# Kernel optimization log

Hardware: AMD Instinct MI355X
Metric: run time of the kernel (lower is better)

Reference implementation:

```python
import jax, jax.numpy as jnp
import numpy as np

B, P, DIN, DK, H = 16, 1024, 768, 768, 12
HD = DK // H
NCLS = 1000


def setup_inputs() -> dict:
    key = jax.random.key(0)
    ks = jax.random.split(key, 7)
    s = 0.02
    return {
        "x": jax.random.normal(ks[0], (B, P, DIN), dtype=jnp.float32),
        "Wqkv": jax.random.normal(ks[1], (DIN, 3 * DK), dtype=jnp.float32) * s,
        "pos": jax.random.normal(ks[2], (1, P, DK), dtype=jnp.float32) * s,
        "Wo": jax.random.normal(ks[3], (DK, DK), dtype=jnp.float32) * s,
        "bo": jax.random.normal(ks[4], (DK,), dtype=jnp.float32) * s,
        "Wc": jax.random.normal(ks[5], (DK, NCLS), dtype=jnp.float32) * s,
        "bc": jax.random.normal(ks[6], (NCLS,), dtype=jnp.float32) * s,
    }


def reference(x, Wqkv, pos, Wo, bo, Wc, bc):
    qkv = x @ Wqkv  # [B,P,3*DK]
    Q, K, V = jnp.split(qkv, 3, axis=-1)
    Q, K, V = Q + pos, K + pos, V + pos

    def heads(t):  # [B,P,DK] -> [B,H,P,HD]
        return t.reshape(B, P, H, HD).transpose(0, 2, 1, 3)

    Q, K, V = heads(Q), heads(K), heads(V)
    scores = jnp.einsum('bhqd,bhkd->bhqk', Q, K) / jnp.sqrt(jnp.float32(HD))
    attn_weights = jax.nn.softmax(scores, axis=-1)
    attn_out = jnp.einsum('bhqk,bhkd->bhqd', attn_weights, V)
    attn_out = attn_out.transpose(0, 2, 1, 3).reshape(B, P, DK)
    attn_out = attn_out @ Wo + bo
    pooled = attn_out.mean(axis=1)  # [B,DK]
    logits = pooled @ Wc + bc
    return logits, attn_weights
```

## Files before the change

### kernel.cpp

```cpp
#include <hip/hip_runtime.h>

#define DI __device__ __forceinline__

typedef float f32x4 __attribute__((ext_vector_type(4)));
typedef unsigned short u16;
typedef u16 u16x8 __attribute__((ext_vector_type(8)));
typedef u16 u16x4 __attribute__((ext_vector_type(4)));
typedef __bf16 bf16x8 __attribute__((ext_vector_type(8)));

DI u16 f2bf(float f) {
    unsigned u = __builtin_bit_cast(unsigned, f);
    u += 0x7fffu + ((u >> 16) & 1u);
    return (u16)(u >> 16);
}

DI float bf2f(u16 b) {
    unsigned u = ((unsigned)b) << 16;
    return __builtin_bit_cast(float, u);
}

DI f32x4 mfma_bf16(u16x8 a, u16x8 b, f32x4 c) {
    return __builtin_amdgcn_mfma_f32_16x16x32_bf16(
        __builtin_bit_cast(bf16x8, a), __builtin_bit_cast(bf16x8, b), c, 0, 0, 0);
}

DI void gload_lds16(const void* g, void* l) {
    __builtin_amdgcn_global_load_lds(
        (const __attribute__((address_space(1))) unsigned int*)g,
        (__attribute__((address_space(3))) unsigned int*)l, 16, 0, 0);
}

DI float fast_exp2(float x) {
    float e;
    asm("v_exp_f32 %0, %1" : "=v"(e) : "v"(x));
    return e;
}

__global__ __launch_bounds__(256) void k_cast_x(const float* __restrict__ x, u16* __restrict__ xb) {
    size_t i = (size_t)blockIdx.x * 256 + threadIdx.x;
    const f32x4* p = (const f32x4*)(x + i * 8);
    f32x4 a = p[0], b = p[1];
    u16x8 o;
    o[0] = f2bf(a[0]); o[1] = f2bf(a[1]); o[2] = f2bf(a[2]); o[3] = f2bf(a[3]);
    o[4] = f2bf(b[0]); o[5] = f2bf(b[1]); o[6] = f2bf(b[2]); o[7] = f2bf(b[3]);
    *(u16x8*)(xb + i * 8) = o;
}

__global__ __launch_bounds__(256) void k_transpose_w(const float* __restrict__ W, u16* __restrict__ Wt) {
    __shared__ float tile[64][65];
    const int t = threadIdx.x;
    const int nb = blockIdx.x * 64, kb = blockIdx.y * 64;
#pragma unroll
    for (int it = 0; it < 4; ++it) {
        int idx = it * 256 + t;
        int kl = idx >> 4, nl4 = (idx & 15) * 4;
        f32x4 v = *(const f32x4*)(W + (size_t)(kb + kl) * 2304 + nb + nl4);
        tile[kl][nl4 + 0] = v[0]; tile[kl][nl4 + 1] = v[1];
        tile[kl][nl4 + 2] = v[2]; tile[kl][nl4 + 3] = v[3];
    }
    __syncthreads();
#pragma unroll
    for (int it = 0; it < 2; ++it) {
        int idx = it * 256 + t;
        int nl = idx >> 3, kc = (idx & 7) * 8;
        u16x8 o;
#pragma unroll
        for (int j = 0; j < 8; ++j) o[j] = f2bf(tile[kc + j][nl]);
        *(u16x8*)(Wt + (size_t)(nb + nl) * 768 + kb + kc) = o;
    }
}

__global__ __launch_bounds__(256, 2) void k_qkv(const u16* __restrict__ A, const u16* __restrict__ Bt,
                                                const float* __restrict__ pos, u16* __restrict__ Qb,
                                                u16* __restrict__ Kb, u16* __restrict__ Vt) {
    __shared__ __align__(16) union SM {
        u16 stage[2][2][8192];
        u16 vt[128][136];
    } sm;
    const int tid = threadIdx.x;
    const int l = tid & 63, w = tid >> 6;
    const int wm = w >> 1, wn = w & 1;
    const int m0 = blockIdx.x * 128, n0 = blockIdx.y * 128;
    const int srow = l >> 3, sslot = (l & 7) ^ srow;
    const int q4 = l >> 4, lr = l & 15;

    f32x4 acc[4][4];
#pragma unroll
    for (int i = 0; i < 4; ++i)
#pragma unroll
        for (int j = 0; j < 4; ++j) acc[i][j] = (f32x4){0.f, 0.f, 0.f, 0.f};

    const size_t abase = (size_t)(m0 + srow) * 768 + sslot * 8;
    const size_t bbase = (size_t)(n0 + srow) * 768 + sslot * 8;

#pragma unroll
    for (int i = 0; i < 4; ++i) {
        int chunk = w * 4 + i;
        gload_lds16(A + abase + (size_t)chunk * 8 * 768, &sm.stage[0][0][chunk * 512]);
        gload_lds16(Bt + bbase + (size_t)chunk * 8 * 768, &sm.stage[0][1][chunk * 512]);
    }
    __syncthreads();

    int cur = 0;
    for (int kt = 0; kt < 12; ++kt) {
        if (kt < 11) {
            const size_t ko = (size_t)(kt + 1) * 64;
#pragma unroll
            for (int i = 0; i < 4; ++i) {
                int chunk = w * 4 + i;
                gload_lds16(A + abase + (size_t)chunk * 8 * 768 + ko, &sm.stage[cur ^ 1][0][chunk * 512]);
                gload_lds16(Bt + bbase + (size_t)chunk * 8 * 768 + ko, &sm.stage[cur ^ 1][1][chunk * 512]);
            }
        }
        const u16* ab = sm.stage[cur][0];
        const u16* bb = sm.stage[cur][1];
        u16x8 af[4][2], bf[4][2];
#pragma unroll
        for (int mi = 0; mi < 4; ++mi) {
            int row = wm * 64 + mi * 16 + lr;
#pragma unroll
            for (int ks = 0; ks < 2; ++ks) {
                int kc = ks * 4 + q4;
                af[mi][ks] = *(const u16x8*)(ab + row * 64 + (kc ^ (row & 7)) * 8);
            }
        }
#pragma unroll
        for (int ni = 0; ni < 4; ++ni) {
            int row = wn * 64 + ni * 16 + lr;
#pragma unroll
            for (int ks = 0; ks < 2; ++ks) {
                int kc = ks * 4 + q4;
                bf[ni][ks] = *(const u16x8*)(bb + row * 64 + (kc ^ (row & 7)) * 8);
            }
        }
#pragma unroll
        for (int mi = 0; mi < 4; ++mi)
#pragma unroll
            for (int ni = 0; ni < 4; ++ni) {
                acc[mi][ni] = mfma_bf16(af[mi][0], bf[ni][0], acc[mi][ni]);
                acc[mi][ni] = mfma_bf16(af[mi][1], bf[ni][1], acc[mi][ni]);
            }
        __syncthreads();
        cur ^= 1;
    }

    const int sec = blockIdx.y / 6;
    const int dsec = n0 - sec * 768;
    const int bidx = m0 >> 10;
    const int prow = m0 & 1023;
    if (sec < 2) {
        u16* outp = sec ? Kb : Qb;
#pragma unroll
        for (int mi = 0; mi < 4; ++mi)
#pragma unroll
            for (int ni = 0; ni < 4; ++ni) {
                const int dl = wn * 64 + ni * 16 + lr;
                const int d = dsec + dl;
#pragma unroll
                for (int r = 0; r < 4; ++r) {
                    const int pl = wm * 64 + mi * 16 + q4 * 4 + r;
                    const int p = prow + pl;
                    sm.vt[pl][dl] = f2bf(acc[mi][ni][r] + pos[p * 768 + d]);
                }
            }
        __syncthreads();
#pragma unroll
        for (int it = 0; it < 8; ++it) {
            const int idx = it * 256 + tid;
            const int pl = idx >> 4, c8 = (idx & 15) * 8;
            u16x8 val = *(const u16x8*)(&sm.vt[pl][c8]);
            const int d = dsec + c8, h = d >> 6, hd = d & 63;
            *(u16x8*)(outp + (size_t)((bidx * 12 + h) * 1024 + prow + pl) * 64 + hd) = val;
        }
    } else {
#pragma unroll
        for (int mi = 0; mi < 4; ++mi)
#pragma unroll
            for (int ni = 0; ni < 4; ++ni) {
                int col = wn * 64 + ni * 16 + lr;
                int d = dsec + col;
                u16x4 pk;
#pragma unroll
                for (int r = 0; r < 4; ++r) {
                    int p = prow + wm * 64 + mi * 16 + q4 * 4 + r;
                    pk[r] = f2bf(acc[mi][ni][r] + pos[p * 768 + d]);
                }
                *(u16x4*)(&sm.vt[col][wm * 64 + mi * 16 + q4 * 4]) = pk;
            }
        __syncthreads();
#pragma unroll
        for (int it = 0; it < 8; ++it) {
            int idx = it * 256 + tid;
            int dl = idx >> 4, c8 = (idx & 15) * 8;
            u16x8 val = *(const u16x8*)(&sm.vt[dl][c8]);
            int d = dsec + dl, h = d >> 6, hd = d & 63;
            *(u16x8*)(Vt + (size_t)((bidx * 12 + h) * 64 + hd) * 1024 + prow + c8) = val;
        }
    }
}

__global__ __launch_bounds__(256, 4) void k_attn(const u16* __restrict__ Qb, const u16* __restrict__ Kb,
                                                 float* __restrict__ Pout, float* __restrict__ csws) {
    __shared__ float stats[64];
    const int tid = threadIdx.x;
    const int l = tid & 63, w = tid >> 6;
    const int lr = l & 15, q4 = l >> 4;
    const int bh = blockIdx.y, qb = blockIdx.x, q0 = qb * 16;
    const u16* Qh = Qb + (size_t)bh * 65536;
    const u16* Kh = Kb + (size_t)bh * 65536;

    u16x8 qf[2];
#pragma unroll
    for (int ks = 0; ks < 2; ++ks)
        qf[ks] = *(const u16x8*)(Qh + (size_t)(q0 + lr) * 64 + ks * 32 + q4 * 8);

    f32x4 acc[16];
#pragma unroll
    for (int nf = 0; nf < 16; ++nf) acc[nf] = (f32x4){0.f, 0.f, 0.f, 0.f};

    const int kc0 = w * 256;
#pragma unroll
    for (int nf = 0; nf < 16; ++nf) {
        const u16* kp = Kh + (size_t)(kc0 + nf * 16 + lr) * 64 + q4 * 8;
        u16x8 kf0 = *(const u16x8*)kp;
        u16x8 kf1 = *(const u16x8*)(kp + 32);
        acc[nf] = mfma_bf16(qf[0], kf0, acc[nf]);
        acc[nf] = mfma_bf16(qf[1], kf1, acc[nf]);
    }

    const float cs = 0.125f * 1.44269504f;
    float inv4[4];
#pragma unroll
    for (int r = 0; r < 4; ++r) {
        float s = 0.f;
#pragma unroll
        for (int nf = 0; nf < 16; ++nf) {
            float e = fast_exp2(acc[nf][r] * cs);
            acc[nf][r] = e;
            s += e;
        }
        s += __shfl_xor(s, 1);
        s += __shfl_xor(s, 2);
        s += __shfl_xor(s, 4);
        s += __shfl_xor(s, 8);
        if (lr == 0) stats[(q4 * 4 + r) * 4 + w] = s;
    }
    __syncthreads();
#pragma unroll
    for (int r = 0; r < 4; ++r) {
        f32x4 s4 = *(const f32x4*)(stats + (q4 * 4 + r) * 4);
        inv4[r] = 1.f / (s4[0] + s4[1] + s4[2] + s4[3]);
    }

    float* Prow = Pout + ((size_t)bh * 1024 + q0) * 1024 + kc0;
    float* crow = csws + ((size_t)(bh * 64 + qb)) * 1024 + kc0;
#pragma unroll
    for (int nf = 0; nf < 16; ++nf) {
        float csum = 0.f;
#pragma unroll
        for (int r = 0; r < 4; ++r) {
            const int row = q4 * 4 + r;
            float p = acc[nf][r] * inv4[r];
            __builtin_nontemporal_store(p, &Prow[(size_t)row * 1024 + nf * 16 + lr]);
            csum += p;
        }
        csum += __shfl_xor(csum, 16);
        csum += __shfl_xor(csum, 32);
        if (l < 16) crow[nf * 16 + l] = csum;
    }
}

__global__ __launch_bounds__(256) void k_pool(const float* __restrict__ csws, const u16* __restrict__ Vt,
                                              float* __restrict__ pooled) {
    __shared__ float cs[1024];
    __shared__ float ps[4][64];
    const int bh = blockIdx.x, t = threadIdx.x;
    f32x4 a = (f32x4){0.f, 0.f, 0.f, 0.f};
    const float* base = csws + (size_t)bh * 64 * 1024 + t * 4;
#pragma unroll 8
    for (int qb = 0; qb < 64; ++qb) a += *(const f32x4*)(base + qb * 1024);
    *(f32x4*)(cs + t * 4) = a;
    __syncthreads();
    const int d = t & 63, kc = t >> 6;
    const u16* vrow = Vt + (size_t)bh * 65536 + (size_t)d * 1024 + kc * 256;
    const float* ck = cs + kc * 256;
    float s = 0.f;
#pragma unroll
    for (int k8 = 0; k8 < 32; ++k8) {
        u16x8 v = *(const u16x8*)(vrow + k8 * 8);
#pragma unroll
        for (int j = 0; j < 8; ++j) s += ck[k8 * 8 + j] * bf2f(v[j]);
    }
    ps[kc][d] = s;
    __syncthreads();
    if (t < 64) {
        const int bb = bh / 12, hh = bh % 12;
        pooled[bb * 768 + hh * 64 + t] = ps[0][t] + ps[1][t] + ps[2][t] + ps[3][t];
    }
}

__global__ __launch_bounds__(128) void k_proj(const float* __restrict__ pooled_sum,
                                              const float* __restrict__ Wo, const float* __restrict__ bo,
                                              float* __restrict__ tmp) {
    const int b = blockIdx.y, j = blockIdx.x * 128 + threadIdx.x;
    __shared__ float pr[768];
    for (int i = threadIdx.x; i < 768; i += 128) pr[i] = pooled_sum[b * 768 + i] * (1.0f / 1024.0f);
    __syncthreads();
    float s = bo[j];
#pragma unroll 4
    for (int d = 0; d < 768; ++d) s = fmaf(pr[d], Wo[d * 768 + j], s);
    tmp[b * 768 + j] = s;
}

__global__ __launch_bounds__(128) void k_cls(const float* __restrict__ tmp,
                                             const float* __restrict__ Wc, const float* __restrict__ bc,
                                             float* __restrict__ out) {
    const int b = blockIdx.y, c = blockIdx.x * 128 + threadIdx.x;
    __shared__ float tr[768];
    for (int i = threadIdx.x; i < 768; i += 128) tr[i] = tmp[b * 768 + i];
    __syncthreads();
    if (c >= 1000) return;
    float s = bc[c];
#pragma unroll 4
    for (int j = 0; j < 768; ++j) s = fmaf(tr[j], Wc[j * 1000 + c], s);
    out[b * 1000 + c] = s;
}

extern "C" void kernel_launch(void* const* d_in, const int* in_sizes, int n_in,
                              void* d_out, int out_size, void* d_ws, size_t ws_size,
                              hipStream_t stream) {
    const float* x    = (const float*)d_in[0];
    const float* Wqkv = (const float*)d_in[1];
    const float* pos  = (const float*)d_in[2];
    const float* Wo   = (const float*)d_in[3];
    const float* bo   = (const float*)d_in[4];
    const float* Wc   = (const float*)d_in[5];
    const float* bc   = (const float*)d_in[6];
    float* out  = (float*)d_out;
    float* attn = out + 16000;

    char* ws = (char*)d_ws;
    u16* xb = (u16*)ws;  ws += (size_t)16384 * 768 * 2;
    u16* Wt = (u16*)ws;  ws += (size_t)2304 * 768 * 2;
    u16* Qb = (u16*)ws;  ws += (size_t)192 * 1024 * 64 * 2;
    u16* Kb = (u16*)ws;  ws += (size_t)192 * 1024 * 64 * 2;
    u16* Vt = (u16*)ws;  ws += (size_t)192 * 1024 * 64 * 2;
    float* csws = (float*)ws;  ws += (size_t)12288 * 1024 * sizeof(float);
    float* pooled = (float*)ws;  ws += 16 * 768 * sizeof(float);
    float* tmp = (float*)ws;

    k_cast_x<<<6144, 256, 0, stream>>>(x, xb);
    k_transpose_w<<<dim3(36, 12), 256, 0, stream>>>(Wqkv, Wt);
    k_qkv<<<dim3(128, 18), 256, 0, stream>>>(xb, Wt, pos, Qb, Kb, Vt);
    k_attn<<<dim3(64, 192), 256, 0, stream>>>(Qb, Kb, attn, csws);
    k_pool<<<192, 256, 0, stream>>>(csws, Vt, pooled);
    k_proj<<<dim3(6, 16), 128, 0, stream>>>(pooled, Wo, bo, tmp);
    k_cls<<<dim3(8, 16), 128, 0, stream>>>(tmp, Wc, bc, out);
}
```

Measured before the change: 447.6 us.

## Recompute QK scores in two passes to cut registers and raise attention occupancy

The attention kernel no longer keeps all 16 score fragments live. It computes QK^T in chunks of four fragments to get the row sums, then recomputes the scores in a second pass and normalizes by subtracting log2(sum) inside the exponent. This lowers register pressure so the launch bound can rise from 4 to 6 blocks per SM, which should help hide the latency of the large P stores. The cost is doubled MFMA work and doubled K loads, with a small change in numerics from the log-domain normalization.

```diff
diff --git a/kernel.cpp b/kernel.cpp
--- a/kernel.cpp
+++ b/kernel.cpp
@@ -33,6 +33,12 @@
 DI float fast_exp2(float x) {
     float e;
     asm("v_exp_f32 %0, %1" : "=v"(e) : "v"(x));
+    return e;
+}
+
+DI float fast_log2(float x) {
+    float e;
+    asm("v_log_f32 %0, %1" : "=v"(e) : "v"(x));
     return e;
 }
 
@@ -199,7 +205,7 @@
     }
 }
 
-__global__ __launch_bounds__(256, 4) void k_attn(const u16* __restrict__ Qb, const u16* __restrict__ Kb,
+__global__ __launch_bounds__(256, 6) void k_attn(const u16* __restrict__ Qb, const u16* __restrict__ Kb,
                                                  float* __restrict__ Pout, float* __restrict__ csws) {
     __shared__ float stats[64];
     const int tid = threadIdx.x;
@@ -208,37 +214,43 @@
     const int bh = blockIdx.y, qb = blockIdx.x, q0 = qb * 16;
     const u16* Qh = Qb + (size_t)bh * 65536;
     const u16* Kh = Kb + (size_t)bh * 65536;
+    const int kc0 = w * 256;
 
     u16x8 qf[2];
 #pragma unroll
     for (int ks = 0; ks < 2; ++ks)
         qf[ks] = *(const u16x8*)(Qh + (size_t)(q0 + lr) * 64 + ks * 32 + q4 * 8);
 
-    f32x4 acc[16];
-#pragma unroll
-    for (int nf = 0; nf < 16; ++nf) acc[nf] = (f32x4){0.f, 0.f, 0.f, 0.f};
-
-    const int kc0 = w * 256;
-#pragma unroll
-    for (int nf = 0; nf < 16; ++nf) {
-        const u16* kp = Kh + (size_t)(kc0 + nf * 16 + lr) * 64 + q4 * 8;
-        u16x8 kf0 = *(const u16x8*)kp;
-        u16x8 kf1 = *(const u16x8*)(kp + 32);
-        acc[nf] = mfma_bf16(qf[0], kf0, acc[nf]);
-        acc[nf] = mfma_bf16(qf[1], kf1, acc[nf]);
-    }
-
     const float cs = 0.125f * 1.44269504f;
-    float inv4[4];
+
+    float s0 = 0.f, s1 = 0.f, s2 = 0.f, s3 = 0.f;
+#pragma unroll
+    for (int c = 0; c < 4; ++c) {
+        f32x4 a4[4];
+#pragma unroll
+        for (int nfl = 0; nfl < 4; ++nfl) a4[nfl] = (f32x4){0.f, 0.f, 0.f, 0.f};
+#pragma unroll
+        for (int nfl = 0; nfl < 4; ++nfl) {
+            const int nf = c * 4 + nfl;
+            const u16* kp = Kh + (size_t)(kc0 + nf * 16 + lr) * 64 + q4 * 8;
+            u16x8 kf0 = *(const u16x8*)kp;
+            u16x8 kf1 = *(const u16x8*)(kp + 32);
+            a4[nfl] = mfma_bf16(qf[0], kf0, a4[nfl]);
+            a4[nfl] = mfma_bf16(qf[1], kf1, a4[nfl]);
+        }
+#pragma unroll
+        for (int nfl = 0; nfl < 4; ++nfl) {
+            s0 += fast_exp2(a4[nfl][0] * cs);
+            s1 += fast_exp2(a4[nfl][1] * cs);
+            s2 += fast_exp2(a4[nfl][2] * cs);
+            s3 += fast_exp2(a4[nfl][3] * cs);
+        }
+    }
+    float sr[4] = {s0, s1, s2, s3};
+    float l2s[4];
 #pragma unroll
     for (int r = 0; r < 4; ++r) {
-        float s = 0.f;
-#pragma unroll
-        for (int nf = 0; nf < 16; ++nf) {
-            float e = fast_exp2(acc[nf][r] * cs);
-            acc[nf][r] = e;
-            s += e;
-        }
+        float s = sr[r];
         s += __shfl_xor(s, 1);
         s += __shfl_xor(s, 2);
         s += __shfl_xor(s, 4);
@@ -249,24 +261,40 @@
 #pragma unroll
     for (int r = 0; r < 4; ++r) {
         f32x4 s4 = *(const f32x4*)(stats + (q4 * 4 + r) * 4);
-        inv4[r] = 1.f / (s4[0] + s4[1] + s4[2] + s4[3]);
+        l2s[r] = fast_log2((s4[0] + s4[1]) + (s4[2] + s4[3]));
     }
 
     float* Prow = Pout + ((size_t)bh * 1024 + q0) * 1024 + kc0;
     float* crow = csws + ((size_t)(bh * 64 + qb)) * 1024 + kc0;
 #pragma unroll
-    for (int nf = 0; nf < 16; ++nf) {
-        float csum = 0.f;
-#pragma unroll
-        for (int r = 0; r < 4; ++r) {
-            const int row = q4 * 4 + r;
-            float p = acc[nf][r] * inv4[r];
-            __builtin_nontemporal_store(p, &Prow[(size_t)row * 1024 + nf * 16 + lr]);
-            csum += p;
-        }
-        csum += __shfl_xor(csum, 16);
-        csum += __shfl_xor(csum, 32);
-        if (l < 16) crow[nf * 16 + l] = csum;
+    for (int c = 0; c < 4; ++c) {
+        f32x4 a4[4];
+#pragma unroll
+        for (int nfl = 0; nfl < 4; ++nfl) a4[nfl] = (f32x4){0.f, 0.f, 0.f, 0.f};
+#pragma unroll
+        for (int nfl = 0; nfl < 4; ++nfl) {
+            const int nf = c * 4 + nfl;
+            const u16* kp = Kh + (size_t)(kc0 + nf * 16 + lr) * 64 + q4 * 8;
+            u16x8 kf0 = *(const u16x8*)kp;
+            u16x8 kf1 = *(const u16x8*)(kp + 32);
+            a4[nfl] = mfma_bf16(qf[0], kf0, a4[nfl]);
+            a4[nfl] = mfma_bf16(qf[1], kf1, a4[nfl]);
+        }
+#pragma unroll
+        for (int nfl = 0; nfl < 4; ++nfl) {
+            const int nf = c * 4 + nfl;
+            float csum = 0.f;
+#pragma unroll
+            for (int r = 0; r < 4; ++r) {
+                const int row = q4 * 4 + r;
+                float p = fast_exp2(fmaf(a4[nfl][r], cs, -l2s[r]));
+                __builtin_nontemporal_store(p, &Prow[(size_t)row * 1024 + nf * 16 + lr]);
+                csum += p;
+            }
+            csum += __shfl_xor(csum, 16);
+            csum += __shfl_xor(csum, 32);
+            if (l < 16) crow[nf * 16 + l] = csum;
+        }
     }
 }
 
```

Measured after the change: 599.2 us. 1.34x slower.
